# Kernel tuning notes

Measured on AMD Instinct MI355X. Metric: run time of the kernel, lower is better.

Reference implementation:

```python
import jax, jax.numpy as jnp
import numpy as np

B, S, D = 4, 2048, 1024

def setup_inputs() -> dict:
    key = jax.random.key(0)
    ks = jax.random.split(key, 4)
    scale = 1.0 / np.sqrt(D)
    return {
        "x": jax.random.normal(ks[0], (B, S, D), dtype=jnp.float32),
        "Wq": jax.random.normal(ks[1], (D, D), dtype=jnp.float32) * scale,
        "bq": jnp.zeros((D,), dtype=jnp.float32),
        "Wk": jax.random.normal(ks[2], (D, D), dtype=jnp.float32) * scale,
        "bk": jnp.zeros((D,), dtype=jnp.float32),
        "Wv": jax.random.normal(ks[3], (D, D), dtype=jnp.float32) * scale,
        "bv": jnp.zeros((D,), dtype=jnp.float32),
    }

def reference(x, Wq, bq, Wk, bk, Wv, bv):
    d = x.shape[-1]
    Q = jnp.einsum('bsd,df->bsf', x, Wq) + bq  # [B,S,D]
    K = jnp.einsum('bsd,df->bsf', x, Wk) + bk
    V = jnp.einsum('bsd,df->bsf', x, Wv) + bv
    scores = jnp.einsum('bqd,bkd->bqk', Q, K) / jnp.sqrt(jnp.asarray(d, x.dtype))  # [B,S,S]
    weights = jax.nn.softmax(scores, axis=-1)
    return jnp.einsum('bqk,bkd->bqd', weights, V)  # [B,S,D]
```

## Files before the change

### kernel.cpp

```cpp
#include <hip/hip_runtime.h>
#include <stdint.h>


typedef __attribute__((ext_vector_type(8))) short bf16x8;
typedef __attribute__((ext_vector_type(4))) float f32x4;
typedef __attribute__((ext_vector_type(4))) unsigned short u16x4;
typedef __attribute__((ext_vector_type(8))) unsigned short u16x8;

__device__ __forceinline__ unsigned short f2bf(float f) {
  union { float f; unsigned u; } v; v.f = f;
  return (unsigned short)((v.u + 0x7FFFu + ((v.u >> 16) & 1u)) >> 16);
}
__device__ __forceinline__ unsigned short f2h(float f) {
  union { _Float16 h; unsigned short u; } v; v.h = (_Float16)f;
  return v.u;
}
__device__ __forceinline__ float h2f(unsigned short u) {
  union { unsigned short u; _Float16 h; } v; v.u = u;
  return (float)v.h;
}

__device__ __forceinline__ void gload16(const void* g, void* l) {
  __builtin_amdgcn_global_load_lds(
      (const __attribute__((address_space(1))) unsigned int*)g,
      (__attribute__((address_space(3))) unsigned int*)l, 16, 0, 0);
}

template <int N>
__device__ __forceinline__ void wait_vm() {
  asm volatile("s_waitcnt vmcnt(%0)" ::"n"(N) : "memory");
}

__device__ __forceinline__ int swz8(int bid, int cpx) {
  return (bid & 7) * cpx + (bid >> 3);
}

__device__ __forceinline__ f32x4 mfma16(bf16x8 a, bf16x8 b, f32x4 c) {
  return __builtin_amdgcn_mfma_f32_16x16x32_bf16(a, b, c, 0, 0, 0);
}

__device__ __forceinline__ void gemm_core2(
    const unsigned short* __restrict__ A, const unsigned short* __restrict__ Bt,
    const int lda, const int ldb, const int nt,
    const long aRow0, const long bRow0, char* lds,
    f32x4 (&acc)[8][4]) {
  constexpr int A_BYTES = 256 * 64;
  constexpr int SLOT = 2 * A_BYTES;
  const int tid = threadIdx.x;
  const int lane = tid & 63;
  const int wid = tid >> 6;
  const int wm = wid >> 2, wn = wid & 3;
  const int l15 = lane & 15, lhi = lane >> 4;

  long goffA[2]; int ldsoffA[2];
#pragma unroll
  for (int j = 0; j < 2; ++j) {
    const int local = j * 8192 + tid * 16;
    const int row = local >> 6, ch = (local >> 4) & 3;
    goffA[j] = (aRow0 + row) * (long)lda + ((ch ^ ((row >> 1) & 3)) << 3);
    ldsoffA[j] = local;
  }
  long goffB[2]; int ldsoffB[2];
#pragma unroll
  for (int j = 0; j < 2; ++j) {
    const int local = j * 8192 + tid * 16;
    const int row = local >> 6, ch = (local >> 4) & 3;
    goffB[j] = (bRow0 + row) * (long)ldb + ((ch ^ ((row >> 1) & 3)) << 3);
    ldsoffB[j] = A_BYTES + local;
  }
  int raddrA[8];
#pragma unroll
  for (int m = 0; m < 8; ++m) {
    const int row = wm * 128 + m * 16 + l15;
    raddrA[m] = row * 64 + ((lhi ^ ((row >> 1) & 3)) << 4);
  }
  int raddrB[4];
#pragma unroll
  for (int n = 0; n < 4; ++n) {
    const int row = wn * 64 + n * 16 + l15;
    raddrB[n] = A_BYTES + row * 64 + ((lhi ^ ((row >> 1) & 3)) << 4);
  }

  const f32x4 z4 = {0.f, 0.f, 0.f, 0.f};
#pragma unroll
  for (int m = 0; m < 8; ++m)
#pragma unroll
    for (int n = 0; n < 4; ++n) acc[m][n] = z4;

  auto stage_A = [&](int T) {
    char* dst = lds + (T % 3) * SLOT;
    const int k0 = T << 5;
#pragma unroll
    for (int j = 0; j < 2; ++j) gload16(A + goffA[j] + k0, dst + ldsoffA[j]);
  };
  auto stage_B = [&](int T) {
    char* dst = lds + (T % 3) * SLOT;
    const int k0 = T << 5;
#pragma unroll
    for (int j = 0; j < 2; ++j) gload16(Bt + goffB[j] + k0, dst + ldsoffB[j]);
  };

  stage_A(0); stage_B(0);
  stage_A(1); stage_B(1);
  wait_vm<4>();
  __builtin_amdgcn_s_barrier();

  for (int t = 0; t < nt; ++t) {
    const char* sb = lds + (t % 3) * SLOT;
    bf16x8 af[4], af2[4], bfr[4];
#pragma unroll
    for (int n = 0; n < 4; ++n) bfr[n] = *(const bf16x8*)(sb + raddrB[n]);
#pragma unroll
    for (int m = 0; m < 4; ++m) af[m] = *(const bf16x8*)(sb + raddrA[m]);
    if (t + 2 < nt) stage_A(t + 2);
    __builtin_amdgcn_s_barrier();
    __builtin_amdgcn_s_setprio(1);
#pragma unroll
    for (int m = 0; m < 4; ++m)
#pragma unroll
      for (int n = 0; n < 4; ++n) acc[m][n] = mfma16(af[m], bfr[n], acc[m][n]);
    __builtin_amdgcn_s_setprio(0);
    __builtin_amdgcn_s_barrier();
#pragma unroll
    for (int m = 0; m < 4; ++m) af2[m] = *(const bf16x8*)(sb + raddrA[4 + m]);
    if (t + 2 < nt) {
      stage_B(t + 2);
      wait_vm<4>();
    } else if (t + 1 < nt) {
      wait_vm<0>();
    }
    __builtin_amdgcn_s_barrier();
    __builtin_amdgcn_s_setprio(1);
#pragma unroll
    for (int m = 0; m < 4; ++m)
#pragma unroll
      for (int n = 0; n < 4; ++n)
        acc[4 + m][n] = mfma16(af2[m], bfr[n], acc[4 + m][n]);
    __builtin_amdgcn_s_setprio(0);
    __builtin_amdgcn_s_barrier();
  }
}

__device__ __forceinline__ void gemm_core(
    const unsigned short* __restrict__ A, const unsigned short* __restrict__ Bt,
    const int lda, const int ldb, const int nt,
    const long aRow0, const long bRow0, char* lds,
    f32x4 (&acc)[8][4]) {
  constexpr int A_BYTES = 256 * 64;
  constexpr int SLOT = A_BYTES + 128 * 64;
  constexpr int LA = 4, LB = 2, L = LA + LB;
  const int tid = threadIdx.x;
  const int lane = tid & 63;
  const int wid = tid >> 6;
  const int wm = wid >> 1, wn = wid & 1;
  const int l15 = lane & 15, lhi = lane >> 4;

  long goffA[LA]; int ldsoffA[LA];
#pragma unroll
  for (int j = 0; j < LA; ++j) {
    const int local = j * 4096 + tid * 16;
    const int row = local >> 6, ch = (local >> 4) & 3;
    goffA[j] = (aRow0 + row) * (long)lda + ((ch ^ ((row >> 1) & 3)) << 3);
    ldsoffA[j] = local;
  }
  long goffB[LB]; int ldsoffB[LB];
#pragma unroll
  for (int j = 0; j < LB; ++j) {
    const int local = j * 4096 + tid * 16;
    const int row = local >> 6, ch = (local >> 4) & 3;
    goffB[j] = (bRow0 + row) * (long)ldb + ((ch ^ ((row >> 1) & 3)) << 3);
    ldsoffB[j] = A_BYTES + local;
  }
  int raddrA[8];
#pragma unroll
  for (int m = 0; m < 8; ++m) {
    const int row = wm * 128 + m * 16 + l15;
    raddrA[m] = row * 64 + ((lhi ^ ((row >> 1) & 3)) << 4);
  }
  int raddrB[4];
#pragma unroll
  for (int n = 0; n < 4; ++n) {
    const int row = wn * 64 + n * 16 + l15;
    raddrB[n] = A_BYTES + row * 64 + ((lhi ^ ((row >> 1) & 3)) << 4);
  }

  const f32x4 z4 = {0.f, 0.f, 0.f, 0.f};
#pragma unroll
  for (int m = 0; m < 8; ++m)
#pragma unroll
    for (int n = 0; n < 4; ++n) acc[m][n] = z4;

  auto stage_tile = [&](int T) {
    char* dst = lds + (T % 3) * SLOT;
    const int k0 = T << 5;
#pragma unroll
    for (int j = 0; j < LA; ++j) gload16(A + goffA[j] + k0, dst + ldsoffA[j]);
#pragma unroll
    for (int j = 0; j < LB; ++j) gload16(Bt + goffB[j] + k0, dst + ldsoffB[j]);
  };

  stage_tile(0);
  stage_tile(1);
  wait_vm<L>();
  __builtin_amdgcn_s_barrier();

  for (int t = 0; t < nt; ++t) {
    const char* sb = lds + (t % 3) * SLOT;
    bf16x8 af[8], bfr[4];
#pragma unroll
    for (int n = 0; n < 4; ++n) bfr[n] = *(const bf16x8*)(sb + raddrB[n]);
#pragma unroll
    for (int m = 0; m < 8; ++m) af[m] = *(const bf16x8*)(sb + raddrA[m]);
    if (t + 2 < nt) stage_tile(t + 2);
    __builtin_amdgcn_s_setprio(1);
#pragma unroll
    for (int m = 0; m < 8; ++m)
#pragma unroll
      for (int n = 0; n < 4; ++n) acc[m][n] = mfma16(af[m], bfr[n], acc[m][n]);
    __builtin_amdgcn_s_setprio(0);
    if (t + 2 < nt) wait_vm<L>();
    else if (t + 1 < nt) wait_vm<0>();
    __builtin_amdgcn_s_barrier();
  }
}

__global__ __launch_bounds__(512, 2) void qkv_kernel(
    const unsigned short* __restrict__ X, const unsigned short* __restrict__ TQ,
    const unsigned short* __restrict__ TK, const unsigned short* __restrict__ TV,
    const float* __restrict__ bq, const float* __restrict__ bk,
    const float* __restrict__ bv, unsigned short* __restrict__ Q16,
    unsigned short* __restrict__ K16, unsigned short* __restrict__ VT) {
  __shared__ char lds[3 * 32768];
  const int wgid = swz8(blockIdx.x, 48);
  const int tm = wgid / 12, tn = wgid % 12;
  const int w = tn >> 2, c = tn & 3;
  const unsigned short* Bt = w == 0 ? TQ : (w == 1 ? TK : TV);
  const float* bias = w == 0 ? bq : (w == 1 ? bk : bv);

  f32x4 acc[8][4];
  gemm_core2(X, Bt, 1024, 1024, 32, (long)tm * 256, (long)c * 256, lds, acc);

  const int tid = threadIdx.x, lane = tid & 63, wid = tid >> 6;
  const int wm = wid >> 2, wn = wid & 3;
  const int l15 = lane & 15, lhi = lane >> 4;
  const int rowBase = tm * 256 + wm * 128;
  const int colBase = c * 256 + wn * 64;
  if (w < 2) {
    unsigned short* C = w == 0 ? Q16 : K16;
#pragma unroll
    for (int m = 0; m < 8; ++m)
#pragma unroll
      for (int n = 0; n < 4; ++n) {
        const int col = colBase + n * 16 + l15;
        const float bvv = bias[col];
#pragma unroll
        for (int j = 0; j < 4; ++j) {
          const int row = rowBase + m * 16 + lhi * 4 + j;
          C[(long)row * 1024 + col] = f2bf(acc[m][n][j] + bvv);
        }
      }
  } else {
#pragma unroll
    for (int m = 0; m < 8; ++m)
#pragma unroll
      for (int n = 0; n < 4; ++n) {
        const int col = colBase + n * 16 + l15;
        const float bvv = bias[col];
        const int row0 = rowBase + m * 16 + lhi * 4;
        const int b = row0 >> 11, s = row0 & 2047;
        u16x4 v;
#pragma unroll
        for (int j = 0; j < 4; ++j) v[j] = f2bf(acc[m][n][j] + bvv);
        *reinterpret_cast<u16x4*>(&VT[(long)b * 2097152 + (long)col * 2048 + s]) = v;
      }
  }
}

__global__ __launch_bounds__(512, 2) void scores_kernel(
    const unsigned short* __restrict__ Q16, const unsigned short* __restrict__ K16,
    unsigned short* __restrict__ SC16) {
  __shared__ char lds[3 * 32768];
  const int wgid = swz8(blockIdx.x, 32);
  const int bz = wgid >> 6, tm = (wgid >> 3) & 7, tn = wgid & 7;
  const unsigned short* A = Q16 + (long)bz * 2097152;
  const unsigned short* Bt = K16 + (long)bz * 2097152;

  f32x4 acc[8][4];
  gemm_core2(A, Bt, 1024, 1024, 32, (long)tm * 256, (long)tn * 256, lds, acc);

  unsigned short* C = SC16 + (long)bz * 4194304;
  const int tid = threadIdx.x, lane = tid & 63, wid = tid >> 6;
  const int wm = wid >> 2, wn = wid & 3;
  const int l15 = lane & 15, lhi = lane >> 4;
  const int rowBase = tm * 256 + wm * 128;
  const int colBase = tn * 256 + wn * 64;
#pragma unroll
  for (int m = 0; m < 8; ++m)
#pragma unroll
    for (int n = 0; n < 4; ++n) {
      const int col = colBase + n * 16 + l15;
#pragma unroll
      for (int j = 0; j < 4; ++j) {
        const int row = rowBase + m * 16 + lhi * 4 + j;
        C[(long)row * 2048 + col] = f2h(acc[m][n][j] * (1.f / 32.f));
      }
    }
}

__global__ __launch_bounds__(256, 2) void pv_kernel(
    const unsigned short* __restrict__ P16, const unsigned short* __restrict__ VT,
    float* __restrict__ out) {
  __shared__ char lds[3 * 24576];
  const int wgid = swz8(blockIdx.x, 32);
  const int bz = wgid >> 6, tm = (wgid >> 3) & 7, tn = wgid & 7;
  const unsigned short* A = P16 + (long)bz * 4194304;
  const unsigned short* Bt = VT + (long)bz * 2097152;

  f32x4 acc[8][4];
  gemm_core(A, Bt, 2048, 2048, 64, (long)tm * 256, (long)tn * 128, lds, acc);

  float* C = out + (long)bz * 2097152;
  const int tid = threadIdx.x, lane = tid & 63, wid = tid >> 6;
  const int wm = wid >> 1, wn = wid & 1;
  const int l15 = lane & 15, lhi = lane >> 4;
  const int rowBase = tm * 256 + wm * 128;
  const int colBase = tn * 128 + wn * 64;
#pragma unroll
  for (int m = 0; m < 8; ++m)
#pragma unroll
    for (int n = 0; n < 4; ++n) {
      const int col = colBase + n * 16 + l15;
#pragma unroll
      for (int j = 0; j < 4; ++j) {
        const int row = rowBase + m * 16 + lhi * 4 + j;
        C[(long)row * 1024 + col] = acc[m][n][j];
      }
    }
}

__global__ __launch_bounds__(256) void cvt4(const float* __restrict__ in,
                                            unsigned short* __restrict__ out) {
  int i = blockIdx.x * 256 + threadIdx.x;
  float4 v = reinterpret_cast<const float4*>(in)[i];
  u16x4 r;
  r[0] = f2bf(v.x); r[1] = f2bf(v.y); r[2] = f2bf(v.z); r[3] = f2bf(v.w);
  reinterpret_cast<u16x4*>(out)[i] = r;
}

__global__ __launch_bounds__(256) void cvtWt(
    const float* __restrict__ w0, const float* __restrict__ w1, const float* __restrict__ w2,
    unsigned short* __restrict__ t0, unsigned short* __restrict__ t1, unsigned short* __restrict__ t2) {
  const float* w = blockIdx.y == 0 ? w0 : (blockIdx.y == 1 ? w1 : w2);
  unsigned short* t = blockIdx.y == 0 ? t0 : (blockIdx.y == 1 ? t1 : t2);
  int id = blockIdx.x * 256 + threadIdx.x;
  int k = id >> 10, n = id & 1023;
  t[n * 1024 + k] = f2bf(w[id]);
}

__global__ __launch_bounds__(256) void softmax_rows(const unsigned short* __restrict__ S,
                                                    unsigned short* __restrict__ P) {
  const long row = blockIdx.x;
  const u16x8* src = reinterpret_cast<const u16x8*>(S + row * 2048);
  const int tid = threadIdx.x;
  u16x8 a = src[tid];
  float v[8];
#pragma unroll
  for (int i = 0; i < 8; ++i) v[i] = h2f(a[i]);
  float m = v[0];
#pragma unroll
  for (int i = 1; i < 8; ++i) m = fmaxf(m, v[i]);
#pragma unroll
  for (int o = 32; o > 0; o >>= 1) m = fmaxf(m, __shfl_xor(m, o));
  __shared__ float red[8];
  const int wid = tid >> 6, lane = tid & 63;
  if (lane == 0) red[wid] = m;
  __syncthreads();
  m = fmaxf(fmaxf(red[0], red[1]), fmaxf(red[2], red[3]));
  float s = 0.f;
#pragma unroll
  for (int i = 0; i < 8; ++i) { v[i] = __expf(v[i] - m); s += v[i]; }
#pragma unroll
  for (int o = 32; o > 0; o >>= 1) s += __shfl_xor(s, o);
  if (lane == 0) red[4 + wid] = s;
  __syncthreads();
  s = (red[4] + red[5]) + (red[6] + red[7]);
  const float inv = 1.f / s;
  u16x8 p;
#pragma unroll
  for (int i = 0; i < 8; ++i) p[i] = f2bf(v[i] * inv);
  reinterpret_cast<u16x8*>(P + row * 2048)[tid] = p;
}

extern "C" void kernel_launch(void* const* d_in, const int* in_sizes, int n_in,
                              void* d_out, int out_size, void* d_ws, size_t ws_size,
                              hipStream_t stream) {
  const float* x  = (const float*)d_in[0];
  const float* Wq = (const float*)d_in[1];
  const float* bq = (const float*)d_in[2];
  const float* Wk = (const float*)d_in[3];
  const float* bk = (const float*)d_in[4];
  const float* Wv = (const float*)d_in[5];
  const float* bv = (const float*)d_in[6];
  float* out = (float*)d_out;

  char* ws = (char*)d_ws;
  const size_t MB = 1024 * 1024;
  unsigned short* X16 = (unsigned short*)(ws);
  unsigned short* TQ  = (unsigned short*)(ws + 16 * MB);
  unsigned short* TK  = (unsigned short*)(ws + 18 * MB);
  unsigned short* TV  = (unsigned short*)(ws + 20 * MB);
  unsigned short* Q16 = (unsigned short*)(ws + 22 * MB);
  unsigned short* K16 = (unsigned short*)(ws + 38 * MB);
  unsigned short* VT  = (unsigned short*)(ws + 54 * MB);
  unsigned short* SC16 = (unsigned short*)(ws + 70 * MB);
  unsigned short* P16 = Q16;

  cvt4<<<8192, 256, 0, stream>>>(x, X16);
  cvtWt<<<dim3(4096, 3), 256, 0, stream>>>(Wq, Wk, Wv, TQ, TK, TV);

  qkv_kernel<<<384, 512, 0, stream>>>(X16, TQ, TK, TV, bq, bk, bv, Q16, K16, VT);
  scores_kernel<<<256, 512, 0, stream>>>(Q16, K16, SC16);
  softmax_rows<<<4 * 2048, 256, 0, stream>>>(SC16, P16);
  pv_kernel<<<256, 256, 0, stream>>>(P16, VT, out);

  (void)in_sizes; (void)n_in; (void)out_size; (void)ws_size;
}
```

Measured before the change: 185.6 us.

## Use K=64 double-buffered GEMM for scores and 256x128 tiles for QKV

Scores GEMM switches to a new core that stages 64-wide K tiles (two 32-wide slices) into double-buffered dynamic LDS of 128 KB. This halves the number of outer iterations and barrier rounds per K, at the cost of one workgroup per CU. The QKV projection moves back to the 256-thread gemm_core with 256x128 tiles and 768 blocks, giving more blocks for better load balance. The change adds a one-time attribute call to allow the larger dynamic shared memory.

```diff
diff --git a/kernel.cpp b/kernel.cpp
--- a/kernel.cpp
+++ b/kernel.cpp
@@ -37,108 +37,6 @@
 
 __device__ __forceinline__ f32x4 mfma16(bf16x8 a, bf16x8 b, f32x4 c) {
   return __builtin_amdgcn_mfma_f32_16x16x32_bf16(a, b, c, 0, 0, 0);
-}
-
-__device__ __forceinline__ void gemm_core2(
-    const unsigned short* __restrict__ A, const unsigned short* __restrict__ Bt,
-    const int lda, const int ldb, const int nt,
-    const long aRow0, const long bRow0, char* lds,
-    f32x4 (&acc)[8][4]) {
-  constexpr int A_BYTES = 256 * 64;
-  constexpr int SLOT = 2 * A_BYTES;
-  const int tid = threadIdx.x;
-  const int lane = tid & 63;
-  const int wid = tid >> 6;
-  const int wm = wid >> 2, wn = wid & 3;
-  const int l15 = lane & 15, lhi = lane >> 4;
-
-  long goffA[2]; int ldsoffA[2];
-#pragma unroll
-  for (int j = 0; j < 2; ++j) {
-    const int local = j * 8192 + tid * 16;
-    const int row = local >> 6, ch = (local >> 4) & 3;
-    goffA[j] = (aRow0 + row) * (long)lda + ((ch ^ ((row >> 1) & 3)) << 3);
-    ldsoffA[j] = local;
-  }
-  long goffB[2]; int ldsoffB[2];
-#pragma unroll
-  for (int j = 0; j < 2; ++j) {
-    const int local = j * 8192 + tid * 16;
-    const int row = local >> 6, ch = (local >> 4) & 3;
-    goffB[j] = (bRow0 + row) * (long)ldb + ((ch ^ ((row >> 1) & 3)) << 3);
-    ldsoffB[j] = A_BYTES + local;
-  }
-  int raddrA[8];
-#pragma unroll
-  for (int m = 0; m < 8; ++m) {
-    const int row = wm * 128 + m * 16 + l15;
-    raddrA[m] = row * 64 + ((lhi ^ ((row >> 1) & 3)) << 4);
-  }
-  int raddrB[4];
-#pragma unroll
-  for (int n = 0; n < 4; ++n) {
-    const int row = wn * 64 + n * 16 + l15;
-    raddrB[n] = A_BYTES + row * 64 + ((lhi ^ ((row >> 1) & 3)) << 4);
-  }
-
-  const f32x4 z4 = {0.f, 0.f, 0.f, 0.f};
-#pragma unroll
-  for (int m = 0; m < 8; ++m)
-#pragma unroll
-    for (int n = 0; n < 4; ++n) acc[m][n] = z4;
-
-  auto stage_A = [&](int T) {
-    char* dst = lds + (T % 3) * SLOT;
-    const int k0 = T << 5;
-#pragma unroll
-    for (int j = 0; j < 2; ++j) gload16(A + goffA[j] + k0, dst + ldsoffA[j]);
-  };
-  auto stage_B = [&](int T) {
-    char* dst = lds + (T % 3) * SLOT;
-    const int k0 = T << 5;
-#pragma unroll
-    for (int j = 0; j < 2; ++j) gload16(Bt + goffB[j] + k0, dst + ldsoffB[j]);
-  };
-
-  stage_A(0); stage_B(0);
-  stage_A(1); stage_B(1);
-  wait_vm<4>();
-  __builtin_amdgcn_s_barrier();
-
-  for (int t = 0; t < nt; ++t) {
-    const char* sb = lds + (t % 3) * SLOT;
-    bf16x8 af[4], af2[4], bfr[4];
-#pragma unroll
-    for (int n = 0; n < 4; ++n) bfr[n] = *(const bf16x8*)(sb + raddrB[n]);
-#pragma unroll
-    for (int m = 0; m < 4; ++m) af[m] = *(const bf16x8*)(sb + raddrA[m]);
-    if (t + 2 < nt) stage_A(t + 2);
-    __builtin_amdgcn_s_barrier();
-    __builtin_amdgcn_s_setprio(1);
-#pragma unroll
-    for (int m = 0; m < 4; ++m)
-#pragma unroll
-      for (int n = 0; n < 4; ++n) acc[m][n] = mfma16(af[m], bfr[n], acc[m][n]);
-    __builtin_amdgcn_s_setprio(0);
-    __builtin_amdgcn_s_barrier();
-#pragma unroll
-    for (int m = 0; m < 4; ++m) af2[m] = *(const bf16x8*)(sb + raddrA[4 + m]);
-    if (t + 2 < nt) {
-      stage_B(t + 2);
-      wait_vm<4>();
-    } else if (t + 1 < nt) {
-      wait_vm<0>();
-    }
-    __builtin_amdgcn_s_barrier();
-    __builtin_amdgcn_s_setprio(1);
-#pragma unroll
-    for (int m = 0; m < 4; ++m)
-#pragma unroll
-      for (int n = 0; n < 4; ++n)
-        acc[4 + m][n] = mfma16(af2[m], bfr[n], acc[4 + m][n]);
-    __builtin_amdgcn_s_setprio(0);
-    __builtin_amdgcn_s_barrier();
-  }
 }
 
 __device__ __forceinline__ void gemm_core(
@@ -224,27 +122,155 @@
   }
 }
 
-__global__ __launch_bounds__(512, 2) void qkv_kernel(
+__device__ __forceinline__ void gemm_core3(
+    const unsigned short* __restrict__ A, const unsigned short* __restrict__ Bt,
+    const int lda, const int ldb, const int nt64,
+    const long aRow0, const long bRow0, char* lds,
+    f32x4 (&acc)[8][4]) {
+  constexpr int SLICE = 256 * 64;
+  constexpr int A_BYTES = 2 * SLICE;
+  constexpr int SLOT = 2 * A_BYTES;
+  const int tid = threadIdx.x;
+  const int lane = tid & 63;
+  const int wid = tid >> 6;
+  const int wm = wid >> 2, wn = wid & 3;
+  const int l15 = lane & 15, lhi = lane >> 4;
+
+  long goffA[2][2], goffB[2][2];
+  int ldsoff[2];
+#pragma unroll
+  for (int j = 0; j < 2; ++j) {
+    const int local = j * 8192 + tid * 16;
+    const int row = local >> 6, ch = (local >> 4) & 3;
+    ldsoff[j] = local;
+    const int kalt = (ch ^ ((row >> 1) & 3)) << 3;
+#pragma unroll
+    for (int kk = 0; kk < 2; ++kk) {
+      goffA[kk][j] = (aRow0 + row) * (long)lda + kk * 32 + kalt;
+      goffB[kk][j] = (bRow0 + row) * (long)ldb + kk * 32 + kalt;
+    }
+  }
+  int raddrA[8];
+#pragma unroll
+  for (int m = 0; m < 8; ++m) {
+    const int row = wm * 128 + m * 16 + l15;
+    raddrA[m] = row * 64 + ((lhi ^ ((row >> 1) & 3)) << 4);
+  }
+  int raddrB[4];
+#pragma unroll
+  for (int n = 0; n < 4; ++n) {
+    const int row = wn * 64 + n * 16 + l15;
+    raddrB[n] = row * 64 + ((lhi ^ ((row >> 1) & 3)) << 4);
+  }
+
+  const f32x4 z4 = {0.f, 0.f, 0.f, 0.f};
+#pragma unroll
+  for (int m = 0; m < 8; ++m)
+#pragma unroll
+    for (int n = 0; n < 4; ++n) acc[m][n] = z4;
+
+  auto stageA = [&](int s, int kk, int T) {
+    char* dst = lds + s * SLOT + kk * SLICE;
+    const long k0 = (long)T << 6;
+#pragma unroll
+    for (int j = 0; j < 2; ++j) gload16(A + goffA[kk][j] + k0, dst + ldsoff[j]);
+  };
+  auto stageB = [&](int s, int kk, int T) {
+    char* dst = lds + s * SLOT + A_BYTES + kk * SLICE;
+    const long k0 = (long)T << 6;
+#pragma unroll
+    for (int j = 0; j < 2; ++j) gload16(Bt + goffB[kk][j] + k0, dst + ldsoff[j]);
+  };
+
+  stageA(0, 0, 0); stageB(0, 0, 0);
+  stageA(0, 1, 0); stageB(0, 1, 0);
+  wait_vm<4>();
+  __builtin_amdgcn_s_barrier();
+
+  int cur = 0;
+  for (int t = 0; t < nt64; ++t) {
+    const char* sb = lds + cur * SLOT;
+    const int nxt = cur ^ 1;
+    const bool pf = (t + 1 < nt64);
+    bf16x8 a0[4], a1[4], b0[4], b1[4];
+#pragma unroll
+    for (int n = 0; n < 4; ++n) b0[n] = *(const bf16x8*)(sb + A_BYTES + raddrB[n]);
+#pragma unroll
+    for (int m = 0; m < 4; ++m) a0[m] = *(const bf16x8*)(sb + raddrA[m]);
+    if (pf) stageA(nxt, 0, t + 1);
+    __builtin_amdgcn_s_barrier();
+    __builtin_amdgcn_s_setprio(1);
+#pragma unroll
+    for (int m = 0; m < 4; ++m)
+#pragma unroll
+      for (int n = 0; n < 4; ++n) acc[m][n] = mfma16(a0[m], b0[n], acc[m][n]);
+    __builtin_amdgcn_s_setprio(0);
+    __builtin_amdgcn_s_barrier();
+#pragma unroll
+    for (int m = 0; m < 4; ++m) a1[m] = *(const bf16x8*)(sb + raddrA[4 + m]);
+    if (pf) { stageB(nxt, 0, t + 1); wait_vm<4>(); }
+    else wait_vm<0>();
+    __builtin_amdgcn_s_barrier();
+    __builtin_amdgcn_s_setprio(1);
+#pragma unroll
+    for (int m = 0; m < 4; ++m)
+#pragma unroll
+      for (int n = 0; n < 4; ++n)
+        acc[4 + m][n] = mfma16(a1[m], b0[n], acc[4 + m][n]);
+    __builtin_amdgcn_s_setprio(0);
+    __builtin_amdgcn_s_barrier();
+#pragma unroll
+    for (int n = 0; n < 4; ++n)
+      b1[n] = *(const bf16x8*)(sb + A_BYTES + SLICE + raddrB[n]);
+#pragma unroll
+    for (int m = 0; m < 4; ++m) a0[m] = *(const bf16x8*)(sb + SLICE + raddrA[m]);
+    if (pf) stageA(nxt, 1, t + 1);
+    __builtin_amdgcn_s_barrier();
+    __builtin_amdgcn_s_setprio(1);
+#pragma unroll
+    for (int m = 0; m < 4; ++m)
+#pragma unroll
+      for (int n = 0; n < 4; ++n) acc[m][n] = mfma16(a0[m], b1[n], acc[m][n]);
+    __builtin_amdgcn_s_setprio(0);
+    __builtin_amdgcn_s_barrier();
+#pragma unroll
+    for (int m = 0; m < 4; ++m)
+      a1[m] = *(const bf16x8*)(sb + SLICE + raddrA[4 + m]);
+    if (pf) { stageB(nxt, 1, t + 1); wait_vm<4>(); }
+    __builtin_amdgcn_s_barrier();
+    __builtin_amdgcn_s_setprio(1);
+#pragma unroll
+    for (int m = 0; m < 4; ++m)
+#pragma unroll
+      for (int n = 0; n < 4; ++n)
+        acc[4 + m][n] = mfma16(a1[m], b1[n], acc[4 + m][n]);
+    __builtin_amdgcn_s_setprio(0);
+    __builtin_amdgcn_s_barrier();
+    cur = nxt;
+  }
+}
+
+__global__ __launch_bounds__(256, 2) void qkv_kernel(
     const unsigned short* __restrict__ X, const unsigned short* __restrict__ TQ,
     const unsigned short* __restrict__ TK, const unsigned short* __restrict__ TV,
     const float* __restrict__ bq, const float* __restrict__ bk,
     const float* __restrict__ bv, unsigned short* __restrict__ Q16,
     unsigned short* __restrict__ K16, unsigned short* __restrict__ VT) {
-  __shared__ char lds[3 * 32768];
-  const int wgid = swz8(blockIdx.x, 48);
-  const int tm = wgid / 12, tn = wgid % 12;
-  const int w = tn >> 2, c = tn & 3;
+  __shared__ char lds[3 * 24576];
+  const int wgid = swz8(blockIdx.x, 96);
+  const int tm = wgid / 24, tn = wgid % 24;
+  const int w = tn >> 3, c = tn & 7;
   const unsigned short* Bt = w == 0 ? TQ : (w == 1 ? TK : TV);
   const float* bias = w == 0 ? bq : (w == 1 ? bk : bv);
 
   f32x4 acc[8][4];
-  gemm_core2(X, Bt, 1024, 1024, 32, (long)tm * 256, (long)c * 256, lds, acc);
+  gemm_core(X, Bt, 1024, 1024, 32, (long)tm * 256, (long)c * 128, lds, acc);
 
   const int tid = threadIdx.x, lane = tid & 63, wid = tid >> 6;
-  const int wm = wid >> 2, wn = wid & 3;
+  const int wm = wid >> 1, wn = wid & 1;
   const int l15 = lane & 15, lhi = lane >> 4;
   const int rowBase = tm * 256 + wm * 128;
-  const int colBase = c * 256 + wn * 64;
+  const int colBase = c * 128 + wn * 64;
   if (w < 2) {
     unsigned short* C = w == 0 ? Q16 : K16;
 #pragma unroll
@@ -276,17 +302,17 @@
   }
 }
 
-__global__ __launch_bounds__(512, 2) void scores_kernel(
+__global__ __launch_bounds__(512, 1) void scores_kernel(
     const unsigned short* __restrict__ Q16, const unsigned short* __restrict__ K16,
     unsigned short* __restrict__ SC16) {
-  __shared__ char lds[3 * 32768];
+  extern __shared__ char lds[];
   const int wgid = swz8(blockIdx.x, 32);
   const int bz = wgid >> 6, tm = (wgid >> 3) & 7, tn = wgid & 7;
   const unsigned short* A = Q16 + (long)bz * 2097152;
   const unsigned short* Bt = K16 + (long)bz * 2097152;
 
   f32x4 acc[8][4];
-  gemm_core2(A, Bt, 1024, 1024, 32, (long)tm * 256, (long)tn * 256, lds, acc);
+  gemm_core3(A, Bt, 1024, 1024, 16, (long)tm * 256, (long)tn * 256, lds, acc);
 
   unsigned short* C = SC16 + (long)bz * 4194304;
   const int tid = threadIdx.x, lane = tid & 63, wid = tid >> 6;
@@ -415,11 +441,18 @@
   unsigned short* SC16 = (unsigned short*)(ws + 70 * MB);
   unsigned short* P16 = Q16;
 
+  static bool attr_set = false;
+  if (!attr_set) {
+    hipFuncSetAttribute(reinterpret_cast<const void*>(scores_kernel),
+                        hipFuncAttributeMaxDynamicSharedMemorySize, 131072);
+    attr_set = true;
+  }
+
   cvt4<<<8192, 256, 0, stream>>>(x, X16);
   cvtWt<<<dim3(4096, 3), 256, 0, stream>>>(Wq, Wk, Wv, TQ, TK, TV);
 
-  qkv_kernel<<<384, 512, 0, stream>>>(X16, TQ, TK, TV, bq, bk, bv, Q16, K16, VT);
-  scores_kernel<<<256, 512, 0, stream>>>(Q16, K16, SC16);
+  qkv_kernel<<<768, 256, 0, stream>>>(X16, TQ, TK, TV, bq, bk, bv, Q16, K16, VT);
+  scores_kernel<<<256, 512, 131072, stream>>>(Q16, K16, SC16);
   softmax_rows<<<4 * 2048, 256, 0, stream>>>(SC16, P16);
   pv_kernel<<<256, 256, 0, stream>>>(P16, VT, out);
 
```

Result: faster. 174.4 us, median of 2 (-6.0%).
